# Optimization experiments

Hardware: AMD Instinct MI355X
Metric: run time of the kernel (lower is better)

## Reference

```python
import jax, jax.numpy as jnp
from jax import lax
import numpy as np

T, B, I, H, L = 512, 256, 512, 256, 2  # seq, batch, input, hidden, layers per stack


def _param_shapes():
    # (stack, layer) -> input dim of that layer. Stack1 layer0 sees I, everything else sees H.
    shapes = []
    for s, in0 in enumerate([I, H]):
        for l in range(L):
            d_in = in0 if l == 0 else H
            shapes.append((f"s{s+1}l{l}", d_in))
    return shapes


def setup_inputs() -> dict:
    key = jax.random.key(0)
    d = {"x": jax.random.normal(jax.random.fold_in(key, 0), (T, B, I), jnp.float32)}
    k = 1.0 / np.sqrt(H)  # pytorch LSTM init scale
    i = 1
    for name, d_in in _param_shapes():
        d[name + "_wih"] = jax.random.uniform(jax.random.fold_in(key, i + 0), (4 * H, d_in), jnp.float32, -k, k)
        d[name + "_whh"] = jax.random.uniform(jax.random.fold_in(key, i + 1), (4 * H, H), jnp.float32, -k, k)
        d[name + "_bih"] = jax.random.uniform(jax.random.fold_in(key, i + 2), (4 * H,), jnp.float32, -k, k)
        d[name + "_bhh"] = jax.random.uniform(jax.random.fold_in(key, i + 3), (4 * H,), jnp.float32, -k, k)
        i += 4
    d["lr_w"] = jax.random.uniform(jax.random.fold_in(key, 100), (H, H), jnp.float32, -k, k)
    d["lr_b"] = jax.random.uniform(jax.random.fold_in(key, 101), (H,), jnp.float32, -k, k)
    return d


def _lstm_layer(x, wih, whh, bih, bhh):
    # x: (T, B, d_in) -> (T, B, H). PyTorch gate order: i, f, g, o.
    xg = jnp.einsum("tbi,gi->tbg", x, wih) + bih + bhh  # precompute input proj (T, B, 4H)
    h0 = jnp.zeros((x.shape[1], H), x.dtype)

    def step(carry, xt):
        h, c = carry
        g = xt + h @ whh.T
        gi, gf, gg, go = jnp.split(g, 4, axis=-1)
        c = jax.nn.sigmoid(gf) * c + jax.nn.sigmoid(gi) * jnp.tanh(gg)
        h = jax.nn.sigmoid(go) * jnp.tanh(c)
        return (h, c), h

    _, ys = lax.scan(step, (h0, h0), xg)
    return ys


def _forward(x, params, lr_w, lr_b):
    out = x
    for (wih, whh, bih, bhh) in params:
        out = _lstm_layer(out, wih, whh, bih, bhh)
    out = out @ lr_w.T + lr_b  # (T, B, H)
    return out[:, -1]  # faithful to original: index dim 1 (batch dim) -> (T, H)


def reference(x,
              s1l0_wih, s1l0_whh, s1l0_bih, s1l0_bhh,
              s1l1_wih, s1l1_whh, s1l1_bih, s1l1_bhh,
              s2l0_wih, s2l0_whh, s2l0_bih, s2l0_bhh,
              s2l1_wih, s2l1_whh, s2l1_bih, s2l1_bhh,
              lr_w, lr_b):
    params = [
        (s1l0_wih, s1l0_whh, s1l0_bih, s1l0_bhh),
        (s1l1_wih, s1l1_whh, s1l1_bih, s1l1_bhh),
        (s2l0_wih, s2l0_whh, s2l0_bih, s2l0_bhh),
        (s2l1_wih, s2l1_whh, s2l1_bih, s2l1_bhh),
    ]
    return _forward(x, params, lr_w, lr_b)
```

## Files before the change

kernel.cpp:

```cpp
#include <hip/hip_runtime.h>
#include <stdint.h>


typedef _Float16 half2v __attribute__((ext_vector_type(2)));

__device__ __forceinline__ float fdot2u(uint32_t w, uint32_t h, float acc) {
#if __has_builtin(__builtin_amdgcn_fdot2)
  return __builtin_amdgcn_fdot2(__builtin_bit_cast(half2v, w),
                                __builtin_bit_cast(half2v, h), acc, false);
#else
  half2v wv = __builtin_bit_cast(half2v, w);
  half2v hv = __builtin_bit_cast(half2v, h);
  acc += (float)wv[0] * (float)hv[0];
  acc += (float)wv[1] * (float)hv[1];
  return acc;
#endif
}

__device__ __forceinline__ float sigmoidf_(float x) {
  return 1.f / (1.f + __expf(-x));
}
__device__ __forceinline__ float tanhf_(float x) {
  return 1.f - 2.f / (__expf(2.f * x) + 1.f);
}

#define CNT_STRIDE 32

__device__ __forceinline__ int cnt_load(const int* p) {
  return __hip_atomic_load(p, __ATOMIC_RELAXED, __HIP_MEMORY_SCOPE_AGENT);
}
__device__ __forceinline__ void cnt_store(int* p, int v) {
  __hip_atomic_store(p, v, __ATOMIC_RELAXED, __HIP_MEMORY_SCOPE_AGENT);
}
__device__ __forceinline__ float ldg_f32(const float* p) {
  uint32_t u = __hip_atomic_load((const uint32_t*)p, __ATOMIC_RELAXED,
                                 __HIP_MEMORY_SCOPE_AGENT);
  return __builtin_bit_cast(float, u);
}
__device__ __forceinline__ void stg_f32(float* p, float v) {
  __hip_atomic_store((uint32_t*)p, __builtin_bit_cast(uint32_t, v),
                     __ATOMIC_RELAXED, __HIP_MEMORY_SCOPE_AGENT);
}
__device__ __forceinline__ uint64_t ldg_u64(const float* p) {
  return __hip_atomic_load((const uint64_t*)p, __ATOMIC_RELAXED,
                           __HIP_MEMORY_SCOPE_AGENT);
}

__device__ __forceinline__ void wait_ge(const int* p, int need, int& rdy) {
  while (rdy < need) {
    rdy = cnt_load(p);
    if (rdy < need) __builtin_amdgcn_s_sleep(2);
  }
  asm volatile("" ::: "memory");
}

__global__ __launch_bounds__(256) void pack_all(
    const float* __restrict__ w0, const float* __restrict__ w1,
    const float* __restrict__ w2, const float* __restrict__ w3,
    const float* __restrict__ w4, const float* __restrict__ w5,
    const float* __restrict__ w6, uint32_t* __restrict__ dst) {
  int b = blockIdx.x;
  int m = b >> 9;
  const float* src = (m == 0) ? w0 : (m == 1) ? w1 : (m == 2) ? w2
                   : (m == 3) ? w3 : (m == 4) ? w4 : (m == 5) ? w5 : w6;
  uint32_t* d = dst + (size_t)m * 131072;
  int idx = (b & 511) * 256 + threadIdx.x;
  int r = idx >> 7, k2 = idx & 127;
  float f0 = src[r * 256 + 2 * k2];
  float f1 = src[r * 256 + 2 * k2 + 1];
  union { _Float16 h; uint16_t u; } a, bb;
  a.h = (_Float16)f0;
  bb.h = (_Float16)f1;
  d[idx] = (uint32_t)a.u | ((uint32_t)bb.u << 16);
}

__global__ __launch_bounds__(256) void proj_gemm(const float* __restrict__ in, int istride, int K,
                                                 const float* __restrict__ W,
                                                 const float* __restrict__ bih,
                                                 const float* __restrict__ bhh,
                                                 float* __restrict__ xg,
                                                 int* __restrict__ cnt) {
  if (blockIdx.x == 0 && blockIdx.y == 0) {
    if (threadIdx.x < 16 * CNT_STRIDE) cnt[threadIdx.x] = 0;
  }
  __shared__ float xs[8][512];
  const int tid = threadIdx.x;
  const int r = blockIdx.x * 256 + tid;
  const int t0 = blockIdx.y * 8;
  for (int tt = 0; tt < 8; ++tt)
    for (int k = tid; k < K; k += 256)
      xs[tt][k] = in[(size_t)(t0 + tt) * istride + k];
  __syncthreads();
  float bias = bih[r] + bhh[r];
  float acc[8];
#pragma unroll
  for (int j = 0; j < 8; ++j) acc[j] = bias;
  const float* wr = W + (size_t)r * K;
  for (int k = 0; k < K; k += 4) {
    float4 w4 = *reinterpret_cast<const float4*>(wr + k);
#pragma unroll
    for (int j = 0; j < 8; ++j)
      acc[j] += xs[j][k] * w4.x + xs[j][k + 1] * w4.y + xs[j][k + 2] * w4.z +
                xs[j][k + 3] * w4.w;
  }
#pragma unroll
  for (int j = 0; j < 8; ++j) xg[(size_t)(t0 + j) * 1024 + r] = acc[j];
}


__device__ void scan_fn(int l, const uint32_t* __restrict__ wpk,
                        const float* __restrict__ xgsrc,
                        float* __restrict__ hseq, int* __restrict__ cnt) {
  __shared__ __align__(16) uint4 wlds[8 * 2 * 512];
  __shared__ __align__(16) uint16_t hbuf[2][256];
  const int tid = threadIdx.x;
  const int j = tid >> 1;
  const int odd = tid & 1;
  const int rA = j + (odd ? 512 : 0);
  const int rB = rA + 256;

  uint32_t wA[96], wB[96];
  {
    const uint4* gA = reinterpret_cast<const uint4*>(wpk + rA * 128);
    const uint4* gB = reinterpret_cast<const uint4*>(wpk + rB * 128);
#pragma unroll
    for (int q = 0; q < 24; ++q) {
      uint4 a = gA[q];
      wA[4 * q + 0] = a.x; wA[4 * q + 1] = a.y; wA[4 * q + 2] = a.z; wA[4 * q + 3] = a.w;
      uint4 b = gB[q];
      wB[4 * q + 0] = b.x; wB[4 * q + 1] = b.y; wB[4 * q + 2] = b.z; wB[4 * q + 3] = b.w;
    }
#pragma unroll
    for (int c = 0; c < 8; ++c) {
      wlds[(c * 2 + 0) * 512 + tid] = gA[24 + c];
      wlds[(c * 2 + 1) * 512 + tid] = gB[24 + c];
    }
  }
  if (tid < 256) hbuf[0][tid] = 0;
  __syncthreads();

  const int* mycnt = &cnt[(4 + (l - 1) * 2 + odd) * CNT_STRIDE];
  int rdy = 0;
  if (l) wait_ge(mycnt, 1, rdy);
  float c_ = 0.f;
  float xga = ldg_f32(xgsrc + rA), xgb = ldg_f32(xgsrc + rB);
  int pp = 0;
  for (int t = 0; t < 512; ++t) {
    const int tn = (t < 511) ? (t + 1) : 511;
    if (l) {
      int need = (t + 2 > 512) ? 512 : (t + 2);
      wait_ge(mycnt, need, rdy);
    }
    float nxa = ldg_f32(xgsrc + tn * 1024 + rA);
    float nxb = ldg_f32(xgsrc + tn * 1024 + rB);

    float accA0 = xga, accA1 = 0.f, accB0 = xgb, accB1 = 0.f;
    const uint4* hv4 = reinterpret_cast<const uint4*>(&hbuf[pp][0]);
#pragma unroll
    for (int ch = 0; ch < 24; ++ch) {
      uint4 h4 = hv4[ch];
      accA0 = fdot2u(wA[4 * ch + 0], h4.x, accA0);
      accA1 = fdot2u(wA[4 * ch + 1], h4.y, accA1);
      accA0 = fdot2u(wA[4 * ch + 2], h4.z, accA0);
      accA1 = fdot2u(wA[4 * ch + 3], h4.w, accA1);
      accB0 = fdot2u(wB[4 * ch + 0], h4.x, accB0);
      accB1 = fdot2u(wB[4 * ch + 1], h4.y, accB1);
      accB0 = fdot2u(wB[4 * ch + 2], h4.z, accB0);
      accB1 = fdot2u(wB[4 * ch + 3], h4.w, accB1);
    }
#pragma unroll
    for (int cc = 0; cc < 8; ++cc) {
      uint4 h4 = hv4[24 + cc];
      uint4 wa = wlds[(cc * 2 + 0) * 512 + tid];
      uint4 wb = wlds[(cc * 2 + 1) * 512 + tid];
      accA0 = fdot2u(wa.x, h4.x, accA0);
      accA1 = fdot2u(wa.y, h4.y, accA1);
      accA0 = fdot2u(wa.z, h4.z, accA0);
      accA1 = fdot2u(wa.w, h4.w, accA1);
      accB0 = fdot2u(wb.x, h4.x, accB0);
      accB1 = fdot2u(wb.y, h4.y, accB1);
      accB0 = fdot2u(wb.z, h4.z, accB0);
      accB1 = fdot2u(wb.w, h4.w, accB1);
    }
    float accA = accA0 + accA1;
    float accB = accB0 + accB1;

    float o0 = __shfl_xor(accA, 1);
    float o1 = __shfl_xor(accB, 1);
    float pi = odd ? o0 : accA;
    float pf = odd ? o1 : accB;
    float pg = odd ? accA : o0;
    float po = odd ? accB : o1;

    c_ = sigmoidf_(pf) * c_ + sigmoidf_(pi) * tanhf_(pg);
    float h = sigmoidf_(po) * tanhf_(c_);
    if (!odd) {
      stg_f32(hseq + t * 256 + j, h);
      union { _Float16 hf; uint16_t u; } cv;
      cv.hf = (_Float16)h;
      hbuf[pp ^ 1][j] = cv.u;
    }
    __syncthreads();
    if (tid == 0) cnt_store(&cnt[l * CNT_STRIDE], t + 1);
    pp ^= 1;
    xga = nxa;
    xgb = nxb;
  }
}

__device__ void proj_fn(int l, int half, const uint32_t* __restrict__ wpk,
                        const float* __restrict__ bih, const float* __restrict__ bhh,
                        const float* __restrict__ hsrc,
                        float* __restrict__ xgdst, int* __restrict__ cnt) {
  __shared__ __align__(16) uint32_t hpk[4][128];
  const int tid = threadIdx.x;
  const int row = half * 512 + tid;

  uint32_t wr_[128];
  {
    const uint4* g = reinterpret_cast<const uint4*>(wpk + (size_t)row * 128);
#pragma unroll
    for (int q = 0; q < 32; ++q) {
      uint4 v = g[q];
      wr_[4 * q + 0] = v.x; wr_[4 * q + 1] = v.y; wr_[4 * q + 2] = v.z; wr_[4 * q + 3] = v.w;
    }
  }
  const float bias = bih[row] + bhh[row];
  const int* prev = &cnt[(l - 1) * CNT_STRIDE];
  int* mine = &cnt[(4 + (l - 1) * 2 + half) * CNT_STRIDE];
  int rdy = 0;
  const int s4 = tid >> 7;
  const int c4 = tid & 127;

  for (int tt = 0; tt < 128; ++tt) {
    const int t0 = tt * 4;
    wait_ge(prev, t0 + 4, rdy);
    {
      uint64_t hv = ldg_u64(hsrc + (t0 + s4) * 256 + 2 * c4);
      float hx = __builtin_bit_cast(float, (uint32_t)hv);
      float hy = __builtin_bit_cast(float, (uint32_t)(hv >> 32));
      union { _Float16 h; uint16_t u; } a, b;
      a.h = (_Float16)hx;
      b.h = (_Float16)hy;
      hpk[s4][c4] = (uint32_t)a.u | ((uint32_t)b.u << 16);
    }
    __syncthreads();
#pragma unroll
    for (int s = 0; s < 4; ++s) {
      float a0 = bias, a1 = 0.f;
      const uint4* hv4 = reinterpret_cast<const uint4*>(hpk[s]);
#pragma unroll
      for (int q = 0; q < 32; ++q) {
        uint4 h4 = hv4[q];
        a0 = fdot2u(wr_[4 * q + 0], h4.x, a0);
        a1 = fdot2u(wr_[4 * q + 1], h4.y, a1);
        a0 = fdot2u(wr_[4 * q + 2], h4.z, a0);
        a1 = fdot2u(wr_[4 * q + 3], h4.w, a1);
      }
      stg_f32(xgdst + (t0 + s) * 1024 + row, a0 + a1);
    }
    __syncthreads();
    if (tid == 0) cnt_store(mine, t0 + 4);
  }
}

__device__ void final_fn(const float* __restrict__ lrw, const float* __restrict__ lrb,
                         const float* __restrict__ h3, float* __restrict__ out,
                         const int* __restrict__ cnt) {
  __shared__ __align__(16) float hs[256];
  const int tid = threadIdx.x;
  const int row = tid >> 1;
  const int kh = tid & 1;
  float w_[128];
  {
    const float4* g = reinterpret_cast<const float4*>(lrw + (size_t)row * 256 + kh * 128);
#pragma unroll
    for (int q = 0; q < 32; ++q) {
      float4 v = g[q];
      w_[4 * q + 0] = v.x; w_[4 * q + 1] = v.y; w_[4 * q + 2] = v.z; w_[4 * q + 3] = v.w;
    }
  }
  const float bias = lrb[row];
  const int* prev = &cnt[3 * CNT_STRIDE];
  int rdy = 0;
  for (int t = 0; t < 512; ++t) {
    wait_ge(prev, t + 1, rdy);
    if (tid < 128) {
      uint64_t hv = ldg_u64(h3 + t * 256 + 2 * tid);
      hs[2 * tid] = __builtin_bit_cast(float, (uint32_t)hv);
      hs[2 * tid + 1] = __builtin_bit_cast(float, (uint32_t)(hv >> 32));
    }
    __syncthreads();
    float a0 = 0.f, a1 = 0.f;
    const float* hp = hs + kh * 128;
#pragma unroll
    for (int k = 0; k < 128; k += 4) {
      a0 += w_[k] * hp[k] + w_[k + 2] * hp[k + 2];
      a1 += w_[k + 1] * hp[k + 1] + w_[k + 3] * hp[k + 3];
    }
    float s = a0 + a1;
    s += __shfl_xor(s, 1);
    if (!kh) out[t * 256 + row] = s + bias;
    __syncthreads();
  }
}

__global__ __launch_bounds__(512, 2) void pipeline(
    const uint32_t* __restrict__ wpkhh, const uint32_t* __restrict__ wpkih,
    const float* __restrict__ xg0, float* __restrict__ xgp,
    float* __restrict__ hseq,
    const float* __restrict__ bih1, const float* __restrict__ bhh1,
    const float* __restrict__ bih2, const float* __restrict__ bhh2,
    const float* __restrict__ bih3, const float* __restrict__ bhh3,
    const float* __restrict__ lrw, const float* __restrict__ lrb,
    float* __restrict__ out, int* __restrict__ cnt) {
  const int bx = blockIdx.x;
  if (bx == 0) {
    scan_fn(0, wpkhh, xg0, hseq, cnt);
  } else if (bx == 10) {
    final_fn(lrw, lrb, hseq + (size_t)3 * 131072, out, cnt);
  } else {
    const int g = bx - 1;
    const int l = g / 3 + 1;
    const int r = g % 3;
    const float* bih = (l == 1) ? bih1 : (l == 2) ? bih2 : bih3;
    const float* bhh = (l == 1) ? bhh1 : (l == 2) ? bhh2 : bhh3;
    if (r < 2)
      proj_fn(l, r, wpkih + (size_t)(l - 1) * 131072, bih, bhh,
              hseq + (size_t)(l - 1) * 131072, xgp + (size_t)(l - 1) * 524288, cnt);
    else
      scan_fn(l, wpkhh + (size_t)l * 131072, xgp + (size_t)(l - 1) * 524288,
              hseq + (size_t)l * 131072, cnt);
  }
}

extern "C" void kernel_launch(void* const* d_in, const int* in_sizes, int n_in,
                              void* d_out, int out_size, void* d_ws, size_t ws_size,
                              hipStream_t stream) {
  (void)in_sizes; (void)n_in; (void)out_size; (void)ws_size;
  const float* x = (const float*)d_in[0];
  const float* wih[4] = {(const float*)d_in[1], (const float*)d_in[5],
                         (const float*)d_in[9], (const float*)d_in[13]};
  const float* whh[4] = {(const float*)d_in[2], (const float*)d_in[6],
                         (const float*)d_in[10], (const float*)d_in[14]};
  const float* bih[4] = {(const float*)d_in[3], (const float*)d_in[7],
                         (const float*)d_in[11], (const float*)d_in[15]};
  const float* bhh[4] = {(const float*)d_in[4], (const float*)d_in[8],
                         (const float*)d_in[12], (const float*)d_in[16]};
  const float* lrw = (const float*)d_in[17];
  const float* lrb = (const float*)d_in[18];
  float* out = (float*)d_out;

  float* ws = (float*)d_ws;
  float* xg0 = ws;
  float* xgp = ws + 524288;
  float* hseq = xgp + 3 * 524288;
  uint32_t* wpkhh = (uint32_t*)(hseq + 4 * 131072);
  uint32_t* wpkih = wpkhh + 4 * 131072;
  int* cnt = (int*)(wpkih + 3 * 131072);

  pack_all<<<3584, 256, 0, stream>>>(whh[0], whh[1], whh[2], whh[3],
                                     wih[1], wih[2], wih[3], wpkhh);

  proj_gemm<<<dim3(4, 64), 256, 0, stream>>>(x + 255 * 512, 256 * 512, 512,
                                             wih[0], bih[0], bhh[0], xg0, cnt);

  pipeline<<<11, 512, 0, stream>>>(wpkhh, wpkih, xg0, xgp, hseq,
                                   bih[1], bhh[1], bih[2], bhh[2], bih[3], bhh[3],
                                   lrw, lrb, out, cnt);
}
```

Before: 1.135 ms.

## Split recurrent dot products over K between thread pairs instead of over gates

Each thread pair now splits the hidden-dimension reduction in half, with each thread computing partial sums for all four gates over 128 hidden elements. It then combines them with four xor-shuffles, instead of each thread owning two full-length gate rows. Each thread still does the same number of dot2 operations, but reads only half of the h vector from shared memory per step, and both threads end up with all gate values. The cost is more shuffles and a different per-thread layout for weights in registers and LDS.

```diff
diff --git a/kernel.cpp b/kernel.cpp
--- a/kernel.cpp
+++ b/kernel.cpp
@@ -111,29 +111,38 @@
 __device__ void scan_fn(int l, const uint32_t* __restrict__ wpk,
                         const float* __restrict__ xgsrc,
                         float* __restrict__ hseq, int* __restrict__ cnt) {
-  __shared__ __align__(16) uint4 wlds[8 * 2 * 512];
+  __shared__ __align__(16) uint4 wlds[16 * 512];
   __shared__ __align__(16) uint16_t hbuf[2][256];
   const int tid = threadIdx.x;
   const int j = tid >> 1;
   const int odd = tid & 1;
   const int rA = j + (odd ? 512 : 0);
   const int rB = rA + 256;
-
-  uint32_t wA[96], wB[96];
+  const int ho = odd * 64;
+
+  uint32_t w0[48], w1[48], w2[48], w3[48];
   {
-    const uint4* gA = reinterpret_cast<const uint4*>(wpk + rA * 128);
-    const uint4* gB = reinterpret_cast<const uint4*>(wpk + rB * 128);
-#pragma unroll
-    for (int q = 0; q < 24; ++q) {
-      uint4 a = gA[q];
-      wA[4 * q + 0] = a.x; wA[4 * q + 1] = a.y; wA[4 * q + 2] = a.z; wA[4 * q + 3] = a.w;
-      uint4 b = gB[q];
-      wB[4 * q + 0] = b.x; wB[4 * q + 1] = b.y; wB[4 * q + 2] = b.z; wB[4 * q + 3] = b.w;
-    }
-#pragma unroll
-    for (int c = 0; c < 8; ++c) {
-      wlds[(c * 2 + 0) * 512 + tid] = gA[24 + c];
-      wlds[(c * 2 + 1) * 512 + tid] = gB[24 + c];
+    const uint4* g0 = reinterpret_cast<const uint4*>(wpk + (size_t)(j)       * 128 + ho);
+    const uint4* g1 = reinterpret_cast<const uint4*>(wpk + (size_t)(j + 256) * 128 + ho);
+    const uint4* g2 = reinterpret_cast<const uint4*>(wpk + (size_t)(j + 512) * 128 + ho);
+    const uint4* g3 = reinterpret_cast<const uint4*>(wpk + (size_t)(j + 768) * 128 + ho);
+#pragma unroll
+    for (int q = 0; q < 12; ++q) {
+      uint4 a = g0[q];
+      w0[4 * q + 0] = a.x; w0[4 * q + 1] = a.y; w0[4 * q + 2] = a.z; w0[4 * q + 3] = a.w;
+      uint4 b = g1[q];
+      w1[4 * q + 0] = b.x; w1[4 * q + 1] = b.y; w1[4 * q + 2] = b.z; w1[4 * q + 3] = b.w;
+      uint4 c = g2[q];
+      w2[4 * q + 0] = c.x; w2[4 * q + 1] = c.y; w2[4 * q + 2] = c.z; w2[4 * q + 3] = c.w;
+      uint4 d = g3[q];
+      w3[4 * q + 0] = d.x; w3[4 * q + 1] = d.y; w3[4 * q + 2] = d.z; w3[4 * q + 3] = d.w;
+    }
+#pragma unroll
+    for (int c = 0; c < 4; ++c) {
+      wlds[(0 * 4 + c) * 512 + tid] = g0[12 + c];
+      wlds[(1 * 4 + c) * 512 + tid] = g1[12 + c];
+      wlds[(2 * 4 + c) * 512 + tid] = g2[12 + c];
+      wlds[(3 * 4 + c) * 512 + tid] = g3[12 + c];
     }
   }
   if (tid < 256) hbuf[0][tid] = 0;
@@ -154,46 +163,64 @@
     float nxa = ldg_f32(xgsrc + tn * 1024 + rA);
     float nxb = ldg_f32(xgsrc + tn * 1024 + rB);
 
-    float accA0 = xga, accA1 = 0.f, accB0 = xgb, accB1 = 0.f;
-    const uint4* hv4 = reinterpret_cast<const uint4*>(&hbuf[pp][0]);
-#pragma unroll
-    for (int ch = 0; ch < 24; ++ch) {
-      uint4 h4 = hv4[ch];
-      accA0 = fdot2u(wA[4 * ch + 0], h4.x, accA0);
-      accA1 = fdot2u(wA[4 * ch + 1], h4.y, accA1);
-      accA0 = fdot2u(wA[4 * ch + 2], h4.z, accA0);
-      accA1 = fdot2u(wA[4 * ch + 3], h4.w, accA1);
-      accB0 = fdot2u(wB[4 * ch + 0], h4.x, accB0);
-      accB1 = fdot2u(wB[4 * ch + 1], h4.y, accB1);
-      accB0 = fdot2u(wB[4 * ch + 2], h4.z, accB0);
-      accB1 = fdot2u(wB[4 * ch + 3], h4.w, accB1);
-    }
-#pragma unroll
-    for (int cc = 0; cc < 8; ++cc) {
-      uint4 h4 = hv4[24 + cc];
-      uint4 wa = wlds[(cc * 2 + 0) * 512 + tid];
-      uint4 wb = wlds[(cc * 2 + 1) * 512 + tid];
-      accA0 = fdot2u(wa.x, h4.x, accA0);
-      accA1 = fdot2u(wa.y, h4.y, accA1);
-      accA0 = fdot2u(wa.z, h4.z, accA0);
-      accA1 = fdot2u(wa.w, h4.w, accA1);
-      accB0 = fdot2u(wb.x, h4.x, accB0);
-      accB1 = fdot2u(wb.y, h4.y, accB1);
-      accB0 = fdot2u(wb.z, h4.z, accB0);
-      accB1 = fdot2u(wb.w, h4.w, accB1);
-    }
-    float accA = accA0 + accA1;
-    float accB = accB0 + accB1;
-
-    float o0 = __shfl_xor(accA, 1);
-    float o1 = __shfl_xor(accB, 1);
-    float pi = odd ? o0 : accA;
-    float pf = odd ? o1 : accB;
-    float pg = odd ? accA : o0;
-    float po = odd ? accB : o1;
-
-    c_ = sigmoidf_(pf) * c_ + sigmoidf_(pi) * tanhf_(pg);
-    float h = sigmoidf_(po) * tanhf_(c_);
+    float a00 = 0.f, a01 = 0.f, a10 = 0.f, a11 = 0.f;
+    float a20 = 0.f, a21 = 0.f, a30 = 0.f, a31 = 0.f;
+    const uint4* hv4 = reinterpret_cast<const uint4*>(&hbuf[pp][odd * 128]);
+#pragma unroll
+    for (int q = 0; q < 12; ++q) {
+      uint4 h4 = hv4[q];
+      a00 = fdot2u(w0[4 * q + 0], h4.x, a00);
+      a01 = fdot2u(w0[4 * q + 1], h4.y, a01);
+      a00 = fdot2u(w0[4 * q + 2], h4.z, a00);
+      a01 = fdot2u(w0[4 * q + 3], h4.w, a01);
+      a10 = fdot2u(w1[4 * q + 0], h4.x, a10);
+      a11 = fdot2u(w1[4 * q + 1], h4.y, a11);
+      a10 = fdot2u(w1[4 * q + 2], h4.z, a10);
+      a11 = fdot2u(w1[4 * q + 3], h4.w, a11);
+      a20 = fdot2u(w2[4 * q + 0], h4.x, a20);
+      a21 = fdot2u(w2[4 * q + 1], h4.y, a21);
+      a20 = fdot2u(w2[4 * q + 2], h4.z, a20);
+      a21 = fdot2u(w2[4 * q + 3], h4.w, a21);
+      a30 = fdot2u(w3[4 * q + 0], h4.x, a30);
+      a31 = fdot2u(w3[4 * q + 1], h4.y, a31);
+      a30 = fdot2u(w3[4 * q + 2], h4.z, a30);
+      a31 = fdot2u(w3[4 * q + 3], h4.w, a31);
+    }
+#pragma unroll
+    for (int c = 0; c < 4; ++c) {
+      uint4 h4 = hv4[12 + c];
+      uint4 v0 = wlds[(0 * 4 + c) * 512 + tid];
+      a00 = fdot2u(v0.x, h4.x, a00);
+      a01 = fdot2u(v0.y, h4.y, a01);
+      a00 = fdot2u(v0.z, h4.z, a00);
+      a01 = fdot2u(v0.w, h4.w, a01);
+      uint4 v1 = wlds[(1 * 4 + c) * 512 + tid];
+      a10 = fdot2u(v1.x, h4.x, a10);
+      a11 = fdot2u(v1.y, h4.y, a11);
+      a10 = fdot2u(v1.z, h4.z, a10);
+      a11 = fdot2u(v1.w, h4.w, a11);
+      uint4 v2 = wlds[(2 * 4 + c) * 512 + tid];
+      a20 = fdot2u(v2.x, h4.x, a20);
+      a21 = fdot2u(v2.y, h4.y, a21);
+      a20 = fdot2u(v2.z, h4.z, a20);
+      a21 = fdot2u(v2.w, h4.w, a21);
+      uint4 v3 = wlds[(3 * 4 + c) * 512 + tid];
+      a30 = fdot2u(v3.x, h4.x, a30);
+      a31 = fdot2u(v3.y, h4.y, a31);
+      a30 = fdot2u(v3.z, h4.z, a30);
+      a31 = fdot2u(v3.w, h4.w, a31);
+    }
+    float p0 = a00 + a01 + (odd ? 0.f : xga);
+    float p1 = a10 + a11 + (odd ? 0.f : xgb);
+    float p2 = a20 + a21 + (odd ? xga : 0.f);
+    float p3 = a30 + a31 + (odd ? xgb : 0.f);
+    float s0 = p0 + __shfl_xor(p0, 1);
+    float s1 = p1 + __shfl_xor(p1, 1);
+    float s2 = p2 + __shfl_xor(p2, 1);
+    float s3 = p3 + __shfl_xor(p3, 1);
+
+    c_ = sigmoidf_(s1) * c_ + sigmoidf_(s0) * tanhf_(s2);
+    float h = sigmoidf_(s3) * tanhf_(c_);
     if (!odd) {
       stg_f32(hseq + t * 256 + j, h);
       union { _Float16 hf; uint16_t u; } cv;
```

After: 1.059 ms. 6.6% less time.
